# Kernel tuning notes

Hardware: AMD Instinct MI355X
Metric: run time of the kernel (lower is better)

Reference implementation:

```python
import jax, jax.numpy as jnp
import numpy as np

N = 100000
E = 3200000
D = 256
HOPS = 3  # K + 1


def setup_inputs() -> dict:
    key = jax.random.key(0)
    k1, k2, k3, k4, k5 = jax.random.split(key, 5)
    node_features = jax.random.normal(k1, (N, D), dtype=jnp.float32)
    # glorot-uniform-like scale for K+1 Dense kernels
    limit = np.sqrt(6.0 / (D + D)).astype(np.float32)
    W = jax.random.uniform(k2, (HOPS, D, D), dtype=jnp.float32, minval=-limit, maxval=limit)
    adj_vals = jax.random.uniform(k3, (HOPS, E), dtype=jnp.float32)
    adj_rows = jax.random.randint(k4, (HOPS, E), 0, N, dtype=jnp.int32)
    adj_cols = jax.random.randint(k5, (HOPS, E), 0, N, dtype=jnp.int32)
    return {"node_features": node_features, "W": W, "adj_vals": adj_vals,
            "adj_rows": adj_rows, "adj_cols": adj_cols}


def reference(node_features, W, adj_vals, adj_rows, adj_cols):
    """Faithful eval-mode forward: sum over hops of SpMM(A_hop, X @ W_hop), then ReLU.
    Dropout is identity at inference (training=False)."""
    n = node_features.shape[0]
    out = jnp.zeros((n, W.shape[-1]), dtype=node_features.dtype)
    for hop in range(W.shape[0]):  # small fixed K+1 loop, structurally distinct hops
        feats = node_features @ W[hop]                      # [N, out_dim]
        msgs = adj_vals[hop][:, None] * feats[adj_cols[hop]]  # gather + scale, [E, out_dim]
        out = out + jax.ops.segment_sum(msgs, adj_rows[hop], num_segments=n)
    return jax.nn.relu(out)
```

## Files before the change

kernel.cpp:

```cpp
#include <hip/hip_runtime.h>

#define D 256
#define MAXB 128
#define PCH 16384

typedef __attribute__((ext_vector_type(8))) short short8;
typedef __attribute__((ext_vector_type(4))) float f32x4;

__device__ __forceinline__ ushort f2b(float f) {
    unsigned u = __float_as_uint(f);
    u += 0x7fffu + ((u >> 16) & 1u);
    return (ushort)(u >> 16);
}
__device__ __forceinline__ float b2f(ushort h) {
    return __uint_as_float(((unsigned)h) << 16);
}
__device__ __forceinline__ long long ntload_ll(const void* p) {
    return __builtin_nontemporal_load((const long long*)p);
}

__global__ void zero_int_kernel(int* __restrict__ p, int n) {
    int stride = gridDim.x * blockDim.x;
    for (int i = blockIdx.x * blockDim.x + threadIdx.x; i < n; i += stride) p[i] = 0;
}

__global__ void xconv_kernel(const float* __restrict__ X, ushort* __restrict__ Xb, int total8) {
    int i = blockIdx.x * 256 + threadIdx.x;
    if (i >= total8) return;
    const float4 a = *(const float4*)(X + (size_t)i * 8);
    const float4 b = *(const float4*)(X + (size_t)i * 8 + 4);
    ushort o8[8] = {f2b(a.x), f2b(a.y), f2b(a.z), f2b(a.w),
                    f2b(b.x), f2b(b.y), f2b(b.z), f2b(b.w)};
    *(short8*)(Xb + (size_t)i * 8) = *(const short8*)o8;
}

__global__ void wconv_kernel(const float* __restrict__ W, ushort* __restrict__ WT, int total) {
    int idx = blockIdx.x * 256 + threadIdx.x;
    if (idx >= total) return;
    int h = idx >> 16;
    int c = (idx >> 8) & 255, k = idx & 255;
    WT[(h << 16) + c * 256 + k] = f2b(W[(h << 16) + k * 256 + c]);
}

__global__ __launch_bounds__(256) void bhist_kernel(const int* __restrict__ rows,
                                                    int* __restrict__ bhistG, int e, int nbuk) {
    __shared__ int lh[MAXB];
    int h = blockIdx.y;
    const int* r = rows + (size_t)h * e;
    for (int k = threadIdx.x; k < nbuk; k += 256) lh[k] = 0;
    __syncthreads();
    int stride = gridDim.x * 256;
    for (int i = blockIdx.x * 256 + threadIdx.x; i < e; i += stride)
        atomicAdd(&lh[r[i] >> 10], 1);
    __syncthreads();
    int* g = bhistG + (size_t)h * nbuk;
    for (int k = threadIdx.x; k < nbuk; k += 256)
        if (lh[k]) atomicAdd(&g[k], lh[k]);
}

__global__ __launch_bounds__(1024) void bscan_kernel(const int* __restrict__ bhistG,
                                                     int* __restrict__ gbase,
                                                     int* __restrict__ gcur, int total) {
    __shared__ int s[1024];
    int t = threadIdx.x;
    int C = (total + 1023) >> 10;
    int i0 = t * C, i1 = min(i0 + C, total);
    int sum = 0;
    for (int i = i0; i < i1; ++i) sum += bhistG[i];
    s[t] = sum;
    __syncthreads();
    for (int off = 1; off < 1024; off <<= 1) {
        int x = (t >= off) ? s[t - off] : 0;
        __syncthreads();
        s[t] += x;
        __syncthreads();
    }
    int run = s[t] - sum;
    for (int i = i0; i < i1; ++i) {
        gbase[i] = run; gcur[i] = run;
        run += bhistG[i];
    }
    if (t == 1023) gbase[total] = s[1023];
}

__global__ __launch_bounds__(512) void bpart_kernel(const int* __restrict__ rows,
                                                    const int* __restrict__ cols,
                                                    const float* __restrict__ vals,
                                                    int* __restrict__ gcur, int2* __restrict__ raw,
                                                    int e, int nbuk) {
    __shared__ int lbase[MAXB];
    __shared__ int lcur[MAXB];
    int h = blockIdx.y;
    const int*   rr = rows + (size_t)h * e;
    const int*   cc = cols + (size_t)h * e;
    const float* vv = vals + (size_t)h * e;
    int c0 = blockIdx.x * PCH;
    int c1 = min(c0 + PCH, e);
    if (c0 >= c1) return;
    for (int k = threadIdx.x; k < nbuk; k += 512) { lbase[k] = 0; lcur[k] = 0; }
    __syncthreads();
    for (int i = c0 + threadIdx.x; i < c1; i += 512)
        atomicAdd(&lbase[rr[i] >> 10], 1);
    __syncthreads();
    int* gc = gcur + (size_t)h * nbuk;
    for (int k = threadIdx.x; k < nbuk; k += 512) {
        int c = lbase[k];
        lbase[k] = c ? atomicAdd(&gc[k], c) : 0;
    }
    __syncthreads();
    for (int i = c0 + threadIdx.x; i < c1; i += 512) {
        int row = rr[i];
        int b = row >> 10;
        int p = lbase[b] + atomicAdd(&lcur[b], 1);
        raw[p] = make_int2(cc[i] | ((row & 1023) << 17), __float_as_int(vv[i]));
    }
}

__global__ __launch_bounds__(512) void bsort_kernel(const int* __restrict__ gbase,
                                                    const int2* __restrict__ raw,
                                                    int2* __restrict__ eg,
                                                    int* __restrict__ row_ptr,
                                                    int n, int nbuk) {
    __shared__ int hist[1024];
    __shared__ int ss[512];
    __shared__ int cur[1024];
    int key = blockIdx.x;
    int h = key / nbuk, b = key % nbuk;
    int s = gbase[key], t = gbase[key + 1];
    int tid = threadIdx.x;
    hist[tid] = 0; hist[tid + 512] = 0;
    __syncthreads();
    for (int i = s + tid; i < t; i += 512)
        atomicAdd(&hist[(((unsigned)raw[i].x) >> 17) & 1023], 1);
    __syncthreads();
    int a = hist[2 * tid], c = hist[2 * tid + 1];
    int pair = a + c;
    ss[tid] = pair;
    __syncthreads();
    for (int off = 1; off < 512; off <<= 1) {
        int x = (tid >= off) ? ss[tid - off] : 0;
        __syncthreads();
        ss[tid] += x;
        __syncthreads();
    }
    int excl = s + ss[tid] - pair;
    cur[2 * tid] = excl;
    cur[2 * tid + 1] = excl + a;
    int* rp = row_ptr + (size_t)h * (n + 1);
    int grow = b * 1024 + 2 * tid;
    if (grow < n)     rp[grow]     = excl;
    if (grow + 1 < n) rp[grow + 1] = excl + a;
    if (tid == 511 && b == nbuk - 1) rp[n] = t;
    __syncthreads();
    for (int i = s + tid; i < t; i += 512) {
        int2 ev = raw[i];
        int j = (((unsigned)ev.x) >> 17) & 1023;
        int p = atomicAdd(&cur[j], 1);
        eg[p] = ev;
    }
}

__global__ __launch_bounds__(256) void spmmX_kernel(const int* __restrict__ rp,
                                                    const int2* __restrict__ eg,
                                                    const ushort* __restrict__ Xb,
                                                    ushort* __restrict__ Yh, int n) {
    int w = threadIdx.x >> 6, lane = threadIdx.x & 63;
    int r = blockIdx.x * 4 + w;
    if (r >= n) return;
    int g = lane >> 4, l4 = lane & 15;
    int doff = l4 * 16;
    const ushort* xb = Xb + doff;
    int e0 = rp[r], e1 = rp[r + 1];
    float acc[16] = {};

    int i0 = e0 + g;
    long long d_cur = (i0 < e1) ? ntload_ll(eg + i0) : 0;
    int c_cur = ((int)(unsigned)d_cur) & 0x1FFFF;
    short8 va = *(const short8*)(xb + (size_t)c_cur * 256);
    short8 vb = *(const short8*)(xb + (size_t)c_cur * 256 + 8);
    int i1 = e0 + 4 + g;
    long long d_nxt = (i1 < e1) ? ntload_ll(eg + i1) : 0;

    for (int ee = e0; ee < e1; ee += 4) {
        int c_nxt = ((int)(unsigned)d_nxt) & 0x1FFFF;
        short8 wa = *(const short8*)(xb + (size_t)c_nxt * 256);
        short8 wb = *(const short8*)(xb + (size_t)c_nxt * 256 + 8);
        int i2 = ee + 8 + g;
        long long d_n2 = (i2 < e1) ? ntload_ll(eg + i2) : 0;

        float val = __int_as_float((int)(d_cur >> 32));
        #pragma unroll
        for (int i = 0; i < 8; ++i)
            acc[i] = fmaf(val, b2f((ushort)va[i]), acc[i]);
        #pragma unroll
        for (int i = 0; i < 8; ++i)
            acc[8 + i] = fmaf(val, b2f((ushort)vb[i]), acc[8 + i]);

        d_cur = d_nxt; va = wa; vb = wb; d_nxt = d_n2;
    }
    #pragma unroll
    for (int i = 0; i < 16; ++i) acc[i] += __shfl_xor(acc[i], 16);
    #pragma unroll
    for (int i = 0; i < 16; ++i) acc[i] += __shfl_xor(acc[i], 32);
    if (g == 0) {
        union { ushort u[16]; long long ll[4]; } o;
        #pragma unroll
        for (int i = 0; i < 16; ++i) o.u[i] = f2b(acc[i]);
        long long* dst = (long long*)(Yh + (size_t)r * 256 + doff);
        __builtin_nontemporal_store(o.ll[0], dst);
        __builtin_nontemporal_store(o.ll[1], dst + 1);
        __builtin_nontemporal_store(o.ll[2], dst + 2);
        __builtin_nontemporal_store(o.ll[3], dst + 3);
    }
}

#define APAD 40

__global__ __launch_bounds__(256) void gemmY_kernel(const ushort* __restrict__ Y,
                                                    const ushort* __restrict__ WT,
                                                    float* __restrict__ out, int M,
                                                    int nh, int mode) {
    __shared__ ushort As[64 * APAD];
    __shared__ ushort Bs[64 * APAD];
    int tid = threadIdx.x;
    int r0 = blockIdx.x * 64, c0 = blockIdx.y * 64;
    int w = tid >> 6, lane = tid & 63;
    int wr = w >> 1, wc = w & 1;
    int lo = lane & 15, hi = lane >> 4;
    f32x4 acc[2][2] = {};
    int srow = tid >> 2;
    int skoff = (tid & 3) * 8;
    int arow = r0 + srow; if (arow > M - 1) arow = M - 1;
    for (int h = 0; h < nh; ++h) {
        const ushort* ap = Y + ((size_t)h * M + arow) * 256 + skoff;
        const ushort* bp = WT + ((size_t)h << 16) + (size_t)(c0 + srow) * 256 + skoff;
        for (int kk = 0; kk < 256; kk += 32) {
            short8 av = *(const short8*)(ap + kk);
            short8 bv = *(const short8*)(bp + kk);
            __syncthreads();
            *(short8*)&As[srow * APAD + skoff] = av;
            *(short8*)&Bs[srow * APAD + skoff] = bv;
            __syncthreads();
            short8 a0 = *(const short8*)&As[(wr * 32 +      lo) * APAD + hi * 8];
            short8 a1 = *(const short8*)&As[(wr * 32 + 16 + lo) * APAD + hi * 8];
            short8 b0 = *(const short8*)&Bs[(wc * 32 +      lo) * APAD + hi * 8];
            short8 b1 = *(const short8*)&Bs[(wc * 32 + 16 + lo) * APAD + hi * 8];
            acc[0][0] = __builtin_amdgcn_mfma_f32_16x16x32_bf16(a0, b0, acc[0][0], 0, 0, 0);
            acc[0][1] = __builtin_amdgcn_mfma_f32_16x16x32_bf16(a0, b1, acc[0][1], 0, 0, 0);
            acc[1][0] = __builtin_amdgcn_mfma_f32_16x16x32_bf16(a1, b0, acc[1][0], 0, 0, 0);
            acc[1][1] = __builtin_amdgcn_mfma_f32_16x16x32_bf16(a1, b1, acc[1][1], 0, 0, 0);
        }
    }
    for (int mi = 0; mi < 2; ++mi)
        for (int ni = 0; ni < 2; ++ni)
            for (int i = 0; i < 4; ++i) {
                int row = r0 + wr * 32 + mi * 16 + hi * 4 + i;
                int col = c0 + wc * 32 + ni * 16 + lo;
                if (row < M) {
                    float v = acc[mi][ni][i];
                    float* op = &out[(size_t)row * 256 + col];
                    if (mode & 1) v += *op;
                    if (mode & 2) v = fmaxf(v, 0.f);
                    *op = v;
                }
            }
}

extern "C" void kernel_launch(void* const* d_in, const int* in_sizes, int n_in,
                              void* d_out, int out_size, void* d_ws, size_t ws_size,
                              hipStream_t stream) {
    const float* X    = (const float*)d_in[0];
    const float* W    = (const float*)d_in[1];
    const float* vals = (const float*)d_in[2];
    const int*   rows = (const int*)d_in[3];
    const int*   cols = (const int*)d_in[4];
    int n    = in_sizes[0] / D;
    int hops = in_sizes[1] / (D * D);
    int e    = in_sizes[2] / hops;

    int nbuk    = (n + 1023) / 1024;
    int nkeytot = hops * nbuk;
    int nchunks = (e + PCH - 1) / PCH;

    float* out = (float*)d_out;

    auto padded = [](size_t b) { return (b + 255) & ~(size_t)255; };
    char* wsb = (char*)d_ws;
    size_t off = 0;
    auto alloc = [&](size_t bytes) -> void* { void* p = wsb + off; off += padded(bytes); return p; };

    ushort* WT      = (ushort*)alloc((size_t)hops * D * D * 2);
    ushort* Xb      = (ushort*)alloc((size_t)n * D * 2);
    int*    bhistG  = (int*)   alloc((size_t)nkeytot * 4);
    int*    gbase   = (int*)   alloc((size_t)(nkeytot + 1) * 4);
    int*    gcur    = (int*)   alloc((size_t)nkeytot * 4);
    int*    row_ptr = (int*)   alloc((size_t)hops * (n + 1) * 4);
    int2*   edges   = (int2*)  alloc((size_t)hops * e * 8);
    size_t  raw_off = off;
    int2*   raw     = (int2*)  alloc((size_t)hops * e * 8);

    bool bigY = (ws_size >= raw_off + (size_t)hops * n * D * 2);
    ushort* Y = (ushort*)raw;

    xconv_kernel<<<(n * D / 8 + 255) / 256, 256, 0, stream>>>(X, Xb, n * D / 8);
    wconv_kernel<<<(hops * D * D + 255) / 256, 256, 0, stream>>>(W, WT, hops * D * D);

    zero_int_kernel<<<(nkeytot + 255) / 256, 256, 0, stream>>>(bhistG, nkeytot);
    bhist_kernel<<<dim3(128, hops), 256, 0, stream>>>(rows, bhistG, e, nbuk);
    bscan_kernel<<<1, 1024, 0, stream>>>(bhistG, gbase, gcur, nkeytot);
    bpart_kernel<<<dim3(nchunks, hops), 512, 0, stream>>>(rows, cols, vals, gcur, raw, e, nbuk);
    bsort_kernel<<<nkeytot, 512, 0, stream>>>(gbase, raw, edges, row_ptr, n, nbuk);

    if (bigY) {
        for (int h = 0; h < hops; ++h)
            spmmX_kernel<<<(n + 3) / 4, 256, 0, stream>>>(row_ptr + (size_t)h * (n + 1), edges,
                                                          Xb, Y + (size_t)h * n * D, n);
        gemmY_kernel<<<dim3((n + 63) / 64, D / 64), 256, 0, stream>>>(Y, WT, out, n, hops, 2);
    } else {
        for (int h = 0; h < hops; ++h) {
            spmmX_kernel<<<(n + 3) / 4, 256, 0, stream>>>(row_ptr + (size_t)h * (n + 1), edges,
                                                          Xb, Y, n);
            int mode = (h > 0 ? 1 : 0) | (h == hops - 1 ? 2 : 0);
            gemmY_kernel<<<dim3((n + 63) / 64, D / 64), 256, 0, stream>>>(Y, WT + (size_t)h * D * D,
                                                                          out, n, 1, mode);
        }
    }
}
```

Measured before the change: 1.136 ms.

## Rework edge partitioning with per-chunk offsets, batch hops, widen GEMM tile

The separate histogram pass and global atomic cursors are replaced by a partition kernel that computes per-chunk bucket offsets locally and writes into chunk-contiguous regions. New sum and scan kernels produce bucket bases, and the sort kernel walks each bucket's runs across all chunks. The SpMM launches for all hops are merged into a single 2D grid. The GEMM now computes full 256-column rows per block, so each A tile is loaded once, at the cost of staging more of B in shared memory per step.

Result: no change. 1.132 ms (-0.4%).

```diff
diff --git a/kernel.cpp b/kernel.cpp
--- a/kernel.cpp
+++ b/kernel.cpp
@@ -2,7 +2,8 @@
 
 #define D 256
 #define MAXB 128
-#define PCH 16384
+#define SR 1024
+#define PCH 32768
 
 typedef __attribute__((ext_vector_type(8))) short short8;
 typedef __attribute__((ext_vector_type(4))) float f32x4;
@@ -17,11 +18,6 @@
 }
 __device__ __forceinline__ long long ntload_ll(const void* p) {
     return __builtin_nontemporal_load((const long long*)p);
-}
-
-__global__ void zero_int_kernel(int* __restrict__ p, int n) {
-    int stride = gridDim.x * blockDim.x;
-    for (int i = blockIdx.x * blockDim.x + threadIdx.x; i < n; i += stride) p[i] = 0;
 }
 
 __global__ void xconv_kernel(const float* __restrict__ X, ushort* __restrict__ Xb, int total8) {
@@ -42,31 +38,72 @@
     WT[(h << 16) + c * 256 + k] = f2b(W[(h << 16) + k * 256 + c]);
 }
 
-__global__ __launch_bounds__(256) void bhist_kernel(const int* __restrict__ rows,
-                                                    int* __restrict__ bhistG, int e, int nbuk) {
+__global__ __launch_bounds__(512) void bpart_kernel(const int* __restrict__ rows,
+                                                    const int* __restrict__ cols,
+                                                    const float* __restrict__ vals,
+                                                    int2* __restrict__ raw,
+                                                    int* __restrict__ runofs,
+                                                    int e, int nbuk, int nch) {
     __shared__ int lh[MAXB];
-    int h = blockIdx.y;
-    const int* r = rows + (size_t)h * e;
-    for (int k = threadIdx.x; k < nbuk; k += 256) lh[k] = 0;
-    __syncthreads();
-    int stride = gridDim.x * 256;
-    for (int i = blockIdx.x * 256 + threadIdx.x; i < e; i += stride)
-        atomicAdd(&lh[r[i] >> 10], 1);
-    __syncthreads();
-    int* g = bhistG + (size_t)h * nbuk;
-    for (int k = threadIdx.x; k < nbuk; k += 256)
-        if (lh[k]) atomicAdd(&g[k], lh[k]);
-}
-
-__global__ __launch_bounds__(1024) void bscan_kernel(const int* __restrict__ bhistG,
-                                                     int* __restrict__ gbase,
-                                                     int* __restrict__ gcur, int total) {
+    __shared__ int lcur[MAXB];
+    int h = blockIdx.y, c = blockIdx.x;
+    int c0 = c * PCH, c1 = min(c0 + PCH, e);
+    if (c0 >= c1) return;
+    const int*   rr = rows + (size_t)h * e;
+    const int*   cc = cols + (size_t)h * e;
+    const float* vv = vals + (size_t)h * e;
+    int tid = threadIdx.x;
+    for (int k = tid; k < nbuk; k += 512) { lh[k] = 0; lcur[k] = 0; }
+    __syncthreads();
+    for (int i = c0 + tid; i < c1; i += 512)
+        atomicAdd(&lh[rr[i] >> 10], 1);
+    __syncthreads();
+    int* ro = runofs + (size_t)(h * nch + c) * (nbuk + 1);
+    if (tid == 0) {
+        int run = h * e + c0;
+        for (int j = 0; j < nbuk; ++j) {
+            ro[j] = run;
+            int v = lh[j];
+            lh[j] = run;
+            run += v;
+        }
+        ro[nbuk] = h * e + c1;
+    }
+    __syncthreads();
+    for (int i = c0 + tid; i < c1; i += 512) {
+        int row = rr[i];
+        int b = row >> 10;
+        int p = lh[b] + atomicAdd(&lcur[b], 1);
+        raw[p] = make_int2(cc[i] | ((row & 1023) << 17), __float_as_int(vv[i]));
+    }
+}
+
+__global__ __launch_bounds__(128) void bsum_kernel(const int* __restrict__ runofs,
+                                                   int* __restrict__ tot, int nbuk, int nch) {
+    int key = blockIdx.x;
+    int h = key / nbuk, b = key % nbuk;
+    int tid = threadIdx.x;
+    int sum = 0;
+    for (int c = tid; c < nch; c += 128) {
+        const int* ro = runofs + (size_t)(h * nch + c) * (nbuk + 1) + b;
+        sum += ro[1] - ro[0];
+    }
+    #pragma unroll
+    for (int o = 32; o > 0; o >>= 1) sum += __shfl_xor(sum, o);
+    __shared__ int ws_[2];
+    if ((tid & 63) == 0) ws_[tid >> 6] = sum;
+    __syncthreads();
+    if (tid == 0) tot[key] = ws_[0] + ws_[1];
+}
+
+__global__ __launch_bounds__(1024) void bscan_kernel(const int* __restrict__ tot,
+                                                     int* __restrict__ gbase, int total) {
     __shared__ int s[1024];
     int t = threadIdx.x;
     int C = (total + 1023) >> 10;
     int i0 = t * C, i1 = min(i0 + C, total);
     int sum = 0;
-    for (int i = i0; i < i1; ++i) sum += bhistG[i];
+    for (int i = i0; i < i1; ++i) sum += tot[i];
     s[t] = sum;
     __syncthreads();
     for (int off = 1; off < 1024; off <<= 1) {
@@ -77,50 +114,18 @@
     }
     int run = s[t] - sum;
     for (int i = i0; i < i1; ++i) {
-        gbase[i] = run; gcur[i] = run;
-        run += bhistG[i];
+        gbase[i] = run;
+        run += tot[i];
     }
     if (t == 1023) gbase[total] = s[1023];
 }
 
-__global__ __launch_bounds__(512) void bpart_kernel(const int* __restrict__ rows,
-                                                    const int* __restrict__ cols,
-                                                    const float* __restrict__ vals,
-                                                    int* __restrict__ gcur, int2* __restrict__ raw,
-                                                    int e, int nbuk) {
-    __shared__ int lbase[MAXB];
-    __shared__ int lcur[MAXB];
-    int h = blockIdx.y;
-    const int*   rr = rows + (size_t)h * e;
-    const int*   cc = cols + (size_t)h * e;
-    const float* vv = vals + (size_t)h * e;
-    int c0 = blockIdx.x * PCH;
-    int c1 = min(c0 + PCH, e);
-    if (c0 >= c1) return;
-    for (int k = threadIdx.x; k < nbuk; k += 512) { lbase[k] = 0; lcur[k] = 0; }
-    __syncthreads();
-    for (int i = c0 + threadIdx.x; i < c1; i += 512)
-        atomicAdd(&lbase[rr[i] >> 10], 1);
-    __syncthreads();
-    int* gc = gcur + (size_t)h * nbuk;
-    for (int k = threadIdx.x; k < nbuk; k += 512) {
-        int c = lbase[k];
-        lbase[k] = c ? atomicAdd(&gc[k], c) : 0;
-    }
-    __syncthreads();
-    for (int i = c0 + threadIdx.x; i < c1; i += 512) {
-        int row = rr[i];
-        int b = row >> 10;
-        int p = lbase[b] + atomicAdd(&lcur[b], 1);
-        raw[p] = make_int2(cc[i] | ((row & 1023) << 17), __float_as_int(vv[i]));
-    }
-}
-
 __global__ __launch_bounds__(512) void bsort_kernel(const int* __restrict__ gbase,
+                                                    const int* __restrict__ runofs,
                                                     const int2* __restrict__ raw,
                                                     int2* __restrict__ eg,
                                                     int* __restrict__ row_ptr,
-                                                    int n, int nbuk) {
+                                                    int n, int nbuk, int nch) {
     __shared__ int hist[1024];
     __shared__ int ss[512];
     __shared__ int cur[1024];
@@ -130,11 +135,15 @@
     int tid = threadIdx.x;
     hist[tid] = 0; hist[tid + 512] = 0;
     __syncthreads();
-    for (int i = s + tid; i < t; i += 512)
-        atomicAdd(&hist[(((unsigned)raw[i].x) >> 17) & 1023], 1);
-    __syncthreads();
-    int a = hist[2 * tid], c = hist[2 * tid + 1];
-    int pair = a + c;
+    for (int c = 0; c < nch; ++c) {
+        const int* ro = runofs + (size_t)(h * nch + c) * (nbuk + 1) + b;
+        int rs = ro[0], re = ro[1];
+        for (int i = rs + tid; i < re; i += 512)
+            atomicAdd(&hist[(((unsigned)raw[i].x) >> 17) & 1023], 1);
+    }
+    __syncthreads();
+    int a = hist[2 * tid], c2 = hist[2 * tid + 1];
+    int pair = a + c2;
     ss[tid] = pair;
     __syncthreads();
     for (int off = 1; off < 512; off <<= 1) {
@@ -147,23 +156,30 @@
     cur[2 * tid] = excl;
     cur[2 * tid + 1] = excl + a;
     int* rp = row_ptr + (size_t)h * (n + 1);
-    int grow = b * 1024 + 2 * tid;
+    int grow = b * SR + 2 * tid;
     if (grow < n)     rp[grow]     = excl;
     if (grow + 1 < n) rp[grow + 1] = excl + a;
-    if (tid == 511 && b == nbuk - 1) rp[n] = t;
-    __syncthreads();
-    for (int i = s + tid; i < t; i += 512) {
-        int2 ev = raw[i];
-        int j = (((unsigned)ev.x) >> 17) & 1023;
-        int p = atomicAdd(&cur[j], 1);
-        eg[p] = ev;
-    }
-}
-
-__global__ __launch_bounds__(256) void spmmX_kernel(const int* __restrict__ rp,
+    if (tid == 0 && b == nbuk - 1) rp[n] = t;
+    __syncthreads();
+    for (int c = 0; c < nch; ++c) {
+        const int* ro = runofs + (size_t)(h * nch + c) * (nbuk + 1) + b;
+        int rs = ro[0], re = ro[1];
+        for (int i = rs + tid; i < re; i += 512) {
+            int2 ev = raw[i];
+            int j = (((unsigned)ev.x) >> 17) & 1023;
+            int p = atomicAdd(&cur[j], 1);
+            eg[p] = ev;
+        }
+    }
+}
+
+__global__ __launch_bounds__(256) void spmmX_kernel(const int* __restrict__ row_ptr,
                                                     const int2* __restrict__ eg,
                                                     const ushort* __restrict__ Xb,
-                                                    ushort* __restrict__ Yh, int n) {
+                                                    ushort* __restrict__ Y, int n,
+                                                    size_t rpStride, size_t yStride) {
+    const int* rp = row_ptr + blockIdx.y * rpStride;
+    ushort* Yh = Y + blockIdx.y * yStride;
     int w = threadIdx.x >> 6, lane = threadIdx.x & 63;
     int r = blockIdx.x * 4 + w;
     if (r >= n) return;
@@ -214,56 +230,60 @@
     }
 }
 
-#define APAD 40
-
-__global__ __launch_bounds__(256) void gemmY_kernel(const ushort* __restrict__ Y,
-                                                    const ushort* __restrict__ WT,
-                                                    float* __restrict__ out, int M,
-                                                    int nh, int mode) {
-    __shared__ ushort As[64 * APAD];
-    __shared__ ushort Bs[64 * APAD];
+#define BP 40
+
+__global__ __launch_bounds__(256) void gemmY2_kernel(const ushort* __restrict__ Y,
+                                                     const ushort* __restrict__ WT,
+                                                     float* __restrict__ out, int M,
+                                                     int nh, int hoff, int mode) {
+    __shared__ ushort As[64 * BP];
+    __shared__ ushort Bs[256 * BP];
     int tid = threadIdx.x;
-    int r0 = blockIdx.x * 64, c0 = blockIdx.y * 64;
+    int r0 = blockIdx.x * 64;
     int w = tid >> 6, lane = tid & 63;
-    int wr = w >> 1, wc = w & 1;
     int lo = lane & 15, hi = lane >> 4;
-    f32x4 acc[2][2] = {};
+    f32x4 acc[16] = {};
+
     int srow = tid >> 2;
-    int skoff = (tid & 3) * 8;
+    int skq = (tid & 3) * 8;
     int arow = r0 + srow; if (arow > M - 1) arow = M - 1;
-    for (int h = 0; h < nh; ++h) {
-        const ushort* ap = Y + ((size_t)h * M + arow) * 256 + skoff;
-        const ushort* bp = WT + ((size_t)h << 16) + (size_t)(c0 + srow) * 256 + skoff;
-        for (int kk = 0; kk < 256; kk += 32) {
-            short8 av = *(const short8*)(ap + kk);
-            short8 bv = *(const short8*)(bp + kk);
-            __syncthreads();
-            *(short8*)&As[srow * APAD + skoff] = av;
-            *(short8*)&Bs[srow * APAD + skoff] = bv;
-            __syncthreads();
-            short8 a0 = *(const short8*)&As[(wr * 32 +      lo) * APAD + hi * 8];
-            short8 a1 = *(const short8*)&As[(wr * 32 + 16 + lo) * APAD + hi * 8];
-            short8 b0 = *(const short8*)&Bs[(wc * 32 +      lo) * APAD + hi * 8];
-            short8 b1 = *(const short8*)&Bs[(wc * 32 + 16 + lo) * APAD + hi * 8];
-            acc[0][0] = __builtin_amdgcn_mfma_f32_16x16x32_bf16(a0, b0, acc[0][0], 0, 0, 0);
-            acc[0][1] = __builtin_amdgcn_mfma_f32_16x16x32_bf16(a0, b1, acc[0][1], 0, 0, 0);
-            acc[1][0] = __builtin_amdgcn_mfma_f32_16x16x32_bf16(a1, b0, acc[1][0], 0, 0, 0);
-            acc[1][1] = __builtin_amdgcn_mfma_f32_16x16x32_bf16(a1, b1, acc[1][1], 0, 0, 0);
-        }
-    }
-    for (int mi = 0; mi < 2; ++mi)
-        for (int ni = 0; ni < 2; ++ni)
-            for (int i = 0; i < 4; ++i) {
-                int row = r0 + wr * 32 + mi * 16 + hi * 4 + i;
-                int col = c0 + wc * 32 + ni * 16 + lo;
-                if (row < M) {
-                    float v = acc[mi][ni][i];
-                    float* op = &out[(size_t)row * 256 + col];
-                    if (mode & 1) v += *op;
-                    if (mode & 2) v = fmaxf(v, 0.f);
-                    *op = v;
-                }
+
+    for (int ks = 0; ks < nh * 8; ++ks) {
+        int hh = ks >> 3, k0 = (ks & 7) * 32;
+        short8 av = *(const short8*)(Y + ((size_t)hh * M + arow) * 256 + k0 + skq);
+        const ushort* bp = WT + ((size_t)(hoff + hh) << 16) + (size_t)tid * 256 + k0;
+        short8 bv0 = *(const short8*)(bp);
+        short8 bv1 = *(const short8*)(bp + 8);
+        short8 bv2 = *(const short8*)(bp + 16);
+        short8 bv3 = *(const short8*)(bp + 24);
+        __syncthreads();
+        *(short8*)&As[srow * BP + skq] = av;
+        *(short8*)&Bs[tid * BP +  0] = bv0;
+        *(short8*)&Bs[tid * BP +  8] = bv1;
+        *(short8*)&Bs[tid * BP + 16] = bv2;
+        *(short8*)&Bs[tid * BP + 24] = bv3;
+        __syncthreads();
+        short8 a = *(const short8*)&As[(w * 16 + lo) * BP + hi * 8];
+        #pragma unroll
+        for (int j = 0; j < 16; ++j) {
+            short8 bf = *(const short8*)&Bs[(j * 16 + lo) * BP + hi * 8];
+            acc[j] = __builtin_amdgcn_mfma_f32_16x16x32_bf16(a, bf, acc[j], 0, 0, 0);
+        }
+    }
+    #pragma unroll
+    for (int j = 0; j < 16; ++j)
+        #pragma unroll
+        for (int i = 0; i < 4; ++i) {
+            int row = r0 + w * 16 + hi * 4 + i;
+            int col = j * 16 + lo;
+            if (row < M) {
+                float v = acc[j][i];
+                float* op = &out[(size_t)row * 256 + col];
+                if (mode & 1) v += *op;
+                if (mode & 2) v = fmaxf(v, 0.f);
+                *op = v;
             }
+        }
 }
 
 extern "C" void kernel_launch(void* const* d_in, const int* in_sizes, int n_in,
@@ -278,9 +298,9 @@
     int hops = in_sizes[1] / (D * D);
     int e    = in_sizes[2] / hops;
 
-    int nbuk    = (n + 1023) / 1024;
+    int nbuk    = (n + SR - 1) / SR;
     int nkeytot = hops * nbuk;
-    int nchunks = (e + PCH - 1) / PCH;
+    int nch     = (e + PCH - 1) / PCH;
 
     float* out = (float*)d_out;
 
@@ -291,9 +311,9 @@
 
     ushort* WT      = (ushort*)alloc((size_t)hops * D * D * 2);
     ushort* Xb      = (ushort*)alloc((size_t)n * D * 2);
-    int*    bhistG  = (int*)   alloc((size_t)nkeytot * 4);
+    int*    runofs  = (int*)   alloc((size_t)hops * nch * (nbuk + 1) * 4);
+    int*    tot     = (int*)   alloc((size_t)nkeytot * 4);
     int*    gbase   = (int*)   alloc((size_t)(nkeytot + 1) * 4);
-    int*    gcur    = (int*)   alloc((size_t)nkeytot * 4);
     int*    row_ptr = (int*)   alloc((size_t)hops * (n + 1) * 4);
     int2*   edges   = (int2*)  alloc((size_t)hops * e * 8);
     size_t  raw_off = off;
@@ -305,24 +325,21 @@
     xconv_kernel<<<(n * D / 8 + 255) / 256, 256, 0, stream>>>(X, Xb, n * D / 8);
     wconv_kernel<<<(hops * D * D + 255) / 256, 256, 0, stream>>>(W, WT, hops * D * D);
 
-    zero_int_kernel<<<(nkeytot + 255) / 256, 256, 0, stream>>>(bhistG, nkeytot);
-    bhist_kernel<<<dim3(128, hops), 256, 0, stream>>>(rows, bhistG, e, nbuk);
-    bscan_kernel<<<1, 1024, 0, stream>>>(bhistG, gbase, gcur, nkeytot);
-    bpart_kernel<<<dim3(nchunks, hops), 512, 0, stream>>>(rows, cols, vals, gcur, raw, e, nbuk);
-    bsort_kernel<<<nkeytot, 512, 0, stream>>>(gbase, raw, edges, row_ptr, n, nbuk);
+    bpart_kernel<<<dim3(nch, hops), 512, 0, stream>>>(rows, cols, vals, raw, runofs, e, nbuk, nch);
+    bsum_kernel<<<nkeytot, 128, 0, stream>>>(runofs, tot, nbuk, nch);
+    bscan_kernel<<<1, 1024, 0, stream>>>(tot, gbase, nkeytot);
+    bsort_kernel<<<nkeytot, 512, 0, stream>>>(gbase, runofs, raw, edges, row_ptr, n, nbuk, nch);
 
     if (bigY) {
-        for (int h = 0; h < hops; ++h)
-            spmmX_kernel<<<(n + 3) / 4, 256, 0, stream>>>(row_ptr + (size_t)h * (n + 1), edges,
-                                                          Xb, Y + (size_t)h * n * D, n);
-        gemmY_kernel<<<dim3((n + 63) / 64, D / 64), 256, 0, stream>>>(Y, WT, out, n, hops, 2);
+        spmmX_kernel<<<dim3((n + 3) / 4, hops), 256, 0, stream>>>(row_ptr, edges, Xb, Y, n,
+                                                                  (size_t)(n + 1), (size_t)n * D);
+        gemmY2_kernel<<<(n + 63) / 64, 256, 0, stream>>>(Y, WT, out, n, hops, 0, 2);
     } else {
         for (int h = 0; h < hops; ++h) {
-            spmmX_kernel<<<(n + 3) / 4, 256, 0, stream>>>(row_ptr + (size_t)h * (n + 1), edges,
-                                                          Xb, Y, n);
+            spmmX_kernel<<<dim3((n + 3) / 4, 1), 256, 0, stream>>>(row_ptr + (size_t)h * (n + 1),
+                                                                   edges, Xb, Y, n, 0, 0);
             int mode = (h > 0 ? 1 : 0) | (h == hops - 1 ? 2 : 0);
-            gemmY_kernel<<<dim3((n + 63) / 64, D / 64), 256, 0, stream>>>(Y, WT + (size_t)h * D * D,
-                                                                          out, n, 1, mode);
-        }
-    }
-}
+            gemmY2_kernel<<<(n + 63) / 64, 256, 0, stream>>>(Y, WT, out, n, 1, h, mode);
+        }
+    }
+}
```
